# Optimization experiments

Hardware: AMD Instinct MI355X
Metric: run time of the kernel (lower is better)

## Reference

```python
import jax, jax.numpy as jnp
import numpy as np

B, S = 16384, 2048
EPS = 1e-8


def _autocorr(x, lag):
    # Pearson correlation between x[:, :-lag] and x[:, lag:] (ddof cancels).
    a = x[:, :-lag]
    b = x[:, lag:]
    am = a.mean(axis=1, keepdims=True)
    bm = b.mean(axis=1, keepdims=True)
    cov = ((a - am) * (b - bm)).mean(axis=1)
    return cov / (a.std(axis=1) * b.std(axis=1))


def _stat_features(x):
    S_len = x.shape[1]
    mean = x.mean(axis=1)
    xc = x - mean[:, None]
    m2 = (xc ** 2).mean(axis=1)
    m3 = (xc ** 3).mean(axis=1)
    m4 = (xc ** 4).mean(axis=1)
    std = jnp.sqrt(m2)
    min_v = x.min(axis=1)
    max_v = x.max(axis=1)
    q = jnp.percentile(x, jnp.array([25.0, 50.0, 75.0]), axis=1)  # [3, B]
    p25, median, p75 = q[0], q[1], q[2]
    diff = jnp.diff(x, axis=1)
    std_diff = diff.std(axis=1)
    trend = std_diff / (std + EPS)
    ac1 = _autocorr(x, 1)
    ac7 = _autocorr(x, 7)
    ac24 = _autocorr(x, 24)
    cv = std / (jnp.abs(mean) + EPS)
    iqr = p75 - p25
    seasonal = x[:, ::24].var(axis=1) / (m2 + EPS)
    skew = m3 / (m2 ** 1.5)          # scipy.stats.skew, bias=True
    kurt = m4 / (m2 ** 2) - 3.0      # scipy.stats.kurtosis, Fisher, bias=True
    length = jnp.full_like(mean, float(S_len))
    sum_abs_diff = jnp.abs(diff).sum(axis=1)
    mean_abs_diff = jnp.abs(diff).mean(axis=1)
    feats = jnp.stack([mean, std, min_v, max_v, median, trend, ac1, ac7, ac24,
                       cv, iqr, seasonal, skew, kurt, length,
                       sum_abs_diff, mean_abs_diff, std_diff, p25, p75], axis=1)
    return jnp.where(jnp.isfinite(feats), feats, 0.0)


def setup_inputs() -> dict:
    key = jax.random.key(0)
    k0, k1, k2, k3, k4 = jax.random.split(key, 5)
    x = jax.random.normal(k0, (B, S), dtype=jnp.float32)
    W1 = jax.random.normal(k1, (64, 20), dtype=jnp.float32) * 0.1
    b1 = jnp.zeros((64,), dtype=jnp.float32)
    W2 = jax.random.normal(k3, (128, 64), dtype=jnp.float32) * 0.1
    b2 = jnp.zeros((128,), dtype=jnp.float32)
    return {"x": x, "W1": W1, "b1": b1, "W2": W2, "b2": b2}


def reference(x, W1, b1, W2, b2):
    feats = _stat_features(x)                      # [B, 20]
    h = jax.nn.relu(feats @ W1.T + b1)             # [B, 64] (dropout inactive at eval)
    return h @ W2.T + b2                           # [B, 128]
```

## Files before the change

kernel.cpp:

```cpp
#include <hip/hip_runtime.h>
#include <cmath>

constexpr int S_LEN = 2048;
constexpr float EPS = 1e-8f;

typedef unsigned uvec32 __attribute__((ext_vector_type(32)));

__device__ __forceinline__ float fin(float v) { return isfinite(v) ? v : 0.0f; }

__device__ __forceinline__ unsigned f2o_bits(unsigned u) {
    return (u & 0x80000000u) ? ~u : (u | 0x80000000u);
}
__device__ __forceinline__ float o2f(unsigned u) {
    return __uint_as_float((u & 0x80000000u) ? (u ^ 0x80000000u) : ~u);
}

template <int Ctrl, int Rmask>
__device__ __forceinline__ int dpp_zero_i(int x) {
    return __builtin_amdgcn_update_dpp(0, x, Ctrl, Rmask, 0xF, true);
}
template <int Ctrl>
__device__ __forceinline__ int dpp_keep_i(int x) {
    return __builtin_amdgcn_update_dpp(x, x, Ctrl, 0xF, 0xF, false);
}
__device__ __forceinline__ int wred_add_i(int v) {
    v += dpp_zero_i<0xB1, 0xF>(v);
    v += dpp_zero_i<0x4E, 0xF>(v);
    v += dpp_zero_i<0x114, 0xF>(v);
    v += dpp_zero_i<0x118, 0xF>(v);
    v += dpp_zero_i<0x142, 0xA>(v);
    v += dpp_zero_i<0x143, 0xC>(v);
    return __builtin_amdgcn_readlane(v, 63);
}
__device__ __forceinline__ float wred_add_f(float v) {
    #define ADDF(CT, RM) v += __uint_as_float((unsigned)dpp_zero_i<CT, RM>((int)__float_as_uint(v)))
    ADDF(0xB1, 0xF); ADDF(0x4E, 0xF); ADDF(0x114, 0xF);
    ADDF(0x118, 0xF); ADDF(0x142, 0xA); ADDF(0x143, 0xC);
    #undef ADDF
    return __uint_as_float((unsigned)__builtin_amdgcn_readlane((int)__float_as_uint(v), 63));
}
__device__ __forceinline__ float wred_min_f(float v) {
    #define MINF(CT) v = fminf(v, __uint_as_float((unsigned)dpp_keep_i<CT>((int)__float_as_uint(v))))
    MINF(0xB1); MINF(0x4E); MINF(0x114); MINF(0x118); MINF(0x142); MINF(0x143);
    #undef MINF
    return __uint_as_float((unsigned)__builtin_amdgcn_readlane((int)__float_as_uint(v), 63));
}
__device__ __forceinline__ float wred_max_f(float v) {
    #define MAXF(CT) v = fmaxf(v, __uint_as_float((unsigned)dpp_keep_i<CT>((int)__float_as_uint(v))))
    MAXF(0xB1); MAXF(0x4E); MAXF(0x114); MAXF(0x118); MAXF(0x142); MAXF(0x143);
    #undef MAXF
    return __uint_as_float((unsigned)__builtin_amdgcn_readlane((int)__float_as_uint(v), 63));
}
__device__ __forceinline__ unsigned wred_umin(unsigned v) {
    #define MINU(CT) { unsigned t = (unsigned)dpp_keep_i<CT>((int)v); v = v < t ? v : t; }
    MINU(0xB1) MINU(0x4E) MINU(0x114) MINU(0x118) MINU(0x142) MINU(0x143)
    #undef MINU
    return (unsigned)__builtin_amdgcn_readlane((int)v, 63);
}
__device__ __forceinline__ float readlane_f(float x, int l) {
    return __uint_as_float((unsigned)__builtin_amdgcn_readlane((int)__float_as_uint(x), l));
}

__device__ __forceinline__ void transpose32(uvec32& A) {
    #pragma unroll
    for (int j = 16; j; j >>= 1) {
        unsigned m = (j == 16) ? 0x0000FFFFu : (j == 8) ? 0x00FF00FFu
                   : (j == 4) ? 0x0F0F0F0Fu : (j == 2) ? 0x33333333u : 0x55555555u;
        #pragma unroll
        for (int k = 0; k < 32; k++) {
            if (!(k & j)) {
                unsigned t = (A[k] ^ (A[k | j] >> j)) & m;
                A[k] = A[k] ^ t;
                A[k | j] = A[k | j] ^ (t << j);
            }
        }
    }
}

#define VF(e) __uint_as_float(a[e])

__global__ __launch_bounds__(256) void transpose_w_kernel(
    const float* __restrict__ W1, const float* __restrict__ W2, float* __restrict__ wt)
{
    int tid = blockIdx.x * blockDim.x + threadIdx.x;
    int stride = gridDim.x * blockDim.x;
    for (int n = tid; n < 64 * 20; n += stride) {
        int j = n & 63, k = n >> 6;
        wt[n] = W1[j * 20 + k];
    }
    for (int n = tid; n < 128 * 64; n += stride) {
        int o = n & 127, k = n >> 7;
        wt[1280 + n] = W2[o * 64 + k];
    }
}

__global__ __launch_bounds__(256) void fused_stats_mlp_kernel(
    const float* __restrict__ x, const float* __restrict__ wt,
    const float* __restrict__ b1, const float* __restrict__ b2,
    float* __restrict__ out, int nrows)
{
    __shared__ __align__(16) float sf[4][20];
    __shared__ __align__(16) float hsh[4][64];

    const int gw   = (blockIdx.x * 256 + threadIdx.x) >> 6;
    const int lane = threadIdx.x & 63;
    const int w    = (threadIdx.x >> 6);
    if (gw >= nrows) return;

    uvec32 a;
    const float* xr = x + (size_t)gw * S_LEN + lane * 32;
    #pragma unroll
    for (int q = 0; q < 8; q++) {
        float4 t = reinterpret_cast<const float4*>(xr)[q];
        a[4 * q + 0] = __float_as_uint(t.x); a[4 * q + 1] = __float_as_uint(t.y);
        a[4 * q + 2] = __float_as_uint(t.z); a[4 * q + 3] = __float_as_uint(t.w);
    }

    float s1 = 0.f, s2 = 0.f, sd2 = 0.f, sad = 0.f;
    float p1 = 0.f, p7 = 0.f, p24 = 0.f, se1 = 0.f, se2 = 0.f;
    float mn = VF(0), mx = VF(0);
    #pragma unroll
    for (int e = 0; e < 32; e++) {
        float val = VF(e);
        s1 += val; s2 = fmaf(val, val, s2);
        mn = fminf(mn, val); mx = fmaxf(mx, val);
    }
    #pragma unroll
    for (int e = 0; e < 31; e++) {
        float d = VF(e + 1) - VF(e);
        sd2 = fmaf(d, d, sd2); sad += fabsf(d);
        p1 = fmaf(VF(e), VF(e + 1), p1);
    }
    #pragma unroll
    for (int e = 0; e < 25; e++) p7 = fmaf(VF(e), VF(e + 7), p7);
    #pragma unroll
    for (int e = 0; e < 8; e++)  p24 = fmaf(VF(e), VF(e + 24), p24);

    const bool notlast = (lane < 63);
    #pragma unroll
    for (int j = 0; j < 24; j++) {
        float nb = __shfl_down(VF(j), 1, 64);
        float g = notlast ? nb : 0.f;
        p24 = fmaf(VF(8 + j), g, p24);
        if (j < 7) p7 = fmaf(VF(25 + j), g, p7);
        if (j == 0 && notlast) {
            float d = nb - VF(31);
            sd2 = fmaf(d, d, sd2); sad += fabsf(d);
            p1 = fmaf(VF(31), nb, p1);
        }
    }
    {
        int r3 = lane % 3;
        float sv = (r3 == 0) ? VF(0) : ((r3 == 1) ? VF(16) : VF(8));
        se1 += sv; se2 = fmaf(sv, sv, se2);
        if (r3 == 0) { se1 += VF(24); se2 = fmaf(VF(24), VF(24), se2); }
    }
    float aa = 0, bb = 0, h7v = 0, hq7v = 0;
    #pragma unroll
    for (int e = 0; e < 24; e++) {
        aa += VF(e); bb = fmaf(VF(e), VF(e), bb);
        if (e == 6) { h7v = aa; hq7v = bb; }
    }
    float cc = 0, dd = 0, t7v = 0, tq7v = 0;
    #pragma unroll
    for (int e = 31; e >= 8; e--) {
        cc += VF(e); dd = fmaf(VF(e), VF(e), dd);
        if (e == 25) { t7v = cc; tq7v = dd; }
    }
    const float h1  = readlane_f(VF(0), 0),   t1  = readlane_f(VF(31), 63);
    const float h7  = readlane_f(h7v, 0),     hq7 = readlane_f(hq7v, 0);
    const float h24 = readlane_f(aa, 0),      hq24 = readlane_f(bb, 0);
    const float t7  = readlane_f(t7v, 63),    tq7 = readlane_f(tq7v, 63);
    const float t24 = readlane_f(cc, 63),     tq24 = readlane_f(dd, 63);
    const float hq1 = h1 * h1, tq1 = t1 * t1;

    float S1  = wred_add_f(s1);
    float mean = S1 * (1.0f / S_LEN);
    float S2  = wred_add_f(s2);
    float SD2 = wred_add_f(sd2);
    float SAD = wred_add_f(sad);
    float P1  = wred_add_f(p1);
    float P7  = wred_add_f(p7);
    float P24 = wred_add_f(p24);
    float SE1 = wred_add_f(se1);
    float SE2 = wred_add_f(se2);
    float MN  = wred_min_f(mn);
    float MX  = wred_max_f(mx);

    float c2 = 0.f, c3 = 0.f, c4 = 0.f;
    #pragma unroll
    for (int e = 0; e < 32; e++) {
        float xc = VF(e) - mean;
        float q = xc * xc;
        c2 += q; c3 = fmaf(q, xc, c3); c4 = fmaf(q, q, c4);
    }
    float C2 = wred_add_f(c2), C3 = wred_add_f(c3), C4 = wred_add_f(c4);

    {
        const float Sf = (float)S_LEN;
        const float nd = Sf - 1.0f;
        float m2v = C2 / Sf, m3v = C3 / Sf, m4v = C4 / Sf;
        float stdv = sqrtf(m2v);
        float dmean = (t1 - h1) / nd;
        float dvar = SD2 / nd - dmean * dmean;
        float std_diff = sqrtf(fmaxf(dvar, 0.f));
        float trend = std_diff / (stdv + EPS);
        float ac[3];
        const float Ls[3] = {1.f, 7.f, 24.f};
        const float Ps[3] = {P1, P7, P24};
        const float hd[3] = {h1, h7, h24},   hqv[3] = {hq1, hq7, hq24};
        const float tl[3] = {t1, t7, t24},   tqv[3] = {tq1, tq7, tq24};
        #pragma unroll
        for (int q = 0; q < 3; q++) {
            float n = Sf - Ls[q];
            float sa = S1 - tl[q], sb = S1 - hd[q];
            float qa = S2 - tqv[q], qb = S2 - hqv[q];
            float am = sa / n, bm = sb / n;
            float cov = Ps[q] / n - am * bm;
            float as_ = sqrtf(fmaxf(qa / n - am * am, 0.f));
            float bs_ = sqrtf(fmaxf(qb / n - bm * bm, 0.f));
            ac[q] = cov / (as_ * bs_);
        }
        float cv = stdv / (fabsf(mean) + EPS);
        float sm = SE1 / 86.f;
        float svar = SE2 / 86.f - sm * sm;
        float seasonal = svar / (m2v + EPS);
        float skew = m3v / (m2v * stdv);
        float kurt = m4v / (m2v * m2v) - 3.f;
        if (lane == 0) {
            float* s = sf[w];
            s[0]  = fin(mean);     s[1]  = fin(stdv);
            s[2]  = fin(MN);       s[3]  = fin(MX);
            s[5]  = fin(trend);    s[6]  = fin(ac[0]);
            s[7]  = fin(ac[1]);    s[8]  = fin(ac[2]);
            s[9]  = fin(cv);       s[11] = fin(seasonal);
            s[12] = fin(skew);     s[13] = fin(kurt);
            s[14] = Sf;            s[15] = fin(SAD);
            s[16] = fin(SAD / nd); s[17] = fin(std_diff);
        }
    }

    #pragma unroll
    for (int e = 0; e < 32; e++) a[e] = f2o_bits(a[e]);
    transpose32(a);

    unsigned act0 = ~0u, act1 = ~0u, act2 = ~0u;
    int K0 = 511, K1 = 1023, K2 = 1535;
    unsigned uK0 = 0, uK1 = 0, uK2 = 0;
    #pragma unroll
    for (int b = 31; b >= 0; b--) {
        unsigned mb = a[31 - b];
        unsigned nmb = ~mb;
        unsigned z0 = act0 & nmb, z1 = act1 & nmb, z2 = act2 & nmb;
        int C01 = wred_add_i(__popc(z0) | (__popc(z1) << 16));
        int Cc2 = wred_add_i(__popc(z2));
        int c0 = C01 & 0xFFFF;
        int c1 = (int)((unsigned)C01 >> 16);
        if (K0 < c0)  act0 = z0; else { K0 -= c0;  act0 &= mb; uK0 |= (1u << b); }
        if (K1 < c1)  act1 = z1; else { K1 -= c1;  act1 &= mb; uK1 |= (1u << b); }
        if (K2 < Cc2) act2 = z2; else { K2 -= Cc2; act2 &= mb; uK2 |= (1u << b); }
    }
    int e01 = wred_add_i(__popc(act0) | (__popc(act1) << 16));
    int eq0 = e01 & 0xFFFF, eq1 = (int)((unsigned)e01 >> 16);
    int eq2 = wred_add_i(__popc(act2));

    transpose32(a);
    unsigned m0 = ~0u, m1 = ~0u, m2 = ~0u;
    #pragma unroll
    for (int e = 0; e < 32; e++) {
        unsigned ue = a[e];
        if (ue > uK0) m0 = m0 < ue ? m0 : ue;
        if (ue > uK1) m1 = m1 < ue ? m1 : ue;
        if (ue > uK2) m2 = m2 < ue ? m2 : ue;
    }
    m0 = wred_umin(m0); m1 = wred_umin(m1); m2 = wred_umin(m2);

    float v511 = o2f(uK0), v1023 = o2f(uK1), v1535 = o2f(uK2);
    float v512  = (K0 + 1 < eq0) ? v511  : o2f(m0);
    float v1024 = (K1 + 1 < eq1) ? v1023 : o2f(m1);
    float v1536 = (K2 + 1 < eq2) ? v1535 : o2f(m2);
    float p25 = v511 + 0.75f * (v512 - v511);
    float med = 0.5f * (v1023 + v1024);
    float p75 = v1535 + 0.25f * (v1536 - v1535);
    float iqr = p75 - p25;

    if (lane == 0) {
        float* s = sf[w];
        s[4]  = fin(med); s[10] = fin(iqr);
        s[18] = fin(p25); s[19] = fin(p75);
    }
    __asm__ volatile("s_waitcnt lgkmcnt(0)" ::: "memory");
    __builtin_amdgcn_sched_barrier(0);

    const float* W1T = wt;
    const float* W2T = wt + 1280;
    const float4* sfv = (const float4*)sf[w];
    float4 f0 = sfv[0], f1 = sfv[1], f2 = sfv[2], f3 = sfv[3], f4 = sfv[4];
    float h = b1[lane];
    h = fmaf(f0.x, W1T[ 0 * 64 + lane], h);
    h = fmaf(f0.y, W1T[ 1 * 64 + lane], h);
    h = fmaf(f0.z, W1T[ 2 * 64 + lane], h);
    h = fmaf(f0.w, W1T[ 3 * 64 + lane], h);
    h = fmaf(f1.x, W1T[ 4 * 64 + lane], h);
    h = fmaf(f1.y, W1T[ 5 * 64 + lane], h);
    h = fmaf(f1.z, W1T[ 6 * 64 + lane], h);
    h = fmaf(f1.w, W1T[ 7 * 64 + lane], h);
    h = fmaf(f2.x, W1T[ 8 * 64 + lane], h);
    h = fmaf(f2.y, W1T[ 9 * 64 + lane], h);
    h = fmaf(f2.z, W1T[10 * 64 + lane], h);
    h = fmaf(f2.w, W1T[11 * 64 + lane], h);
    h = fmaf(f3.x, W1T[12 * 64 + lane], h);
    h = fmaf(f3.y, W1T[13 * 64 + lane], h);
    h = fmaf(f3.z, W1T[14 * 64 + lane], h);
    h = fmaf(f3.w, W1T[15 * 64 + lane], h);
    h = fmaf(f4.x, W1T[16 * 64 + lane], h);
    h = fmaf(f4.y, W1T[17 * 64 + lane], h);
    h = fmaf(f4.z, W1T[18 * 64 + lane], h);
    h = fmaf(f4.w, W1T[19 * 64 + lane], h);
    h = fmaxf(h, 0.f);
    hsh[w][lane] = h;
    __asm__ volatile("s_waitcnt lgkmcnt(0)" ::: "memory");
    __builtin_amdgcn_sched_barrier(0);

    const int j2 = lane * 2;
    float2 b2v = *(const float2*)(b2 + j2);
    float acc0 = b2v.x, acc1 = b2v.y;
    const float4* hv4 = (const float4*)hsh[w];
    #pragma unroll
    for (int q = 0; q < 16; q++) {
        float4 hq = hv4[q];
        const float* wp = W2T + (4 * q) * 128 + j2;
        float2 w0 = *(const float2*)(wp);
        float2 w1 = *(const float2*)(wp + 128);
        float2 w2 = *(const float2*)(wp + 256);
        float2 w3 = *(const float2*)(wp + 384);
        acc0 = fmaf(hq.x, w0.x, acc0); acc1 = fmaf(hq.x, w0.y, acc1);
        acc0 = fmaf(hq.y, w1.x, acc0); acc1 = fmaf(hq.y, w1.y, acc1);
        acc0 = fmaf(hq.z, w2.x, acc0); acc1 = fmaf(hq.z, w2.y, acc1);
        acc0 = fmaf(hq.w, w3.x, acc0); acc1 = fmaf(hq.w, w3.y, acc1);
    }
    *(float2*)(out + (size_t)gw * 128 + j2) = make_float2(acc0, acc1);
}

extern "C" void kernel_launch(void* const* d_in, const int* in_sizes, int n_in,
                              void* d_out, int out_size, void* d_ws, size_t ws_size,
                              hipStream_t stream) {
    const float* x  = (const float*)d_in[0];
    const float* W1 = (const float*)d_in[1];
    const float* b1 = (const float*)d_in[2];
    const float* W2 = (const float*)d_in[3];
    const float* b2 = (const float*)d_in[4];
    float* out = (float*)d_out;
    float* wt  = (float*)d_ws;
    int nrows = in_sizes[0] / S_LEN;
    int blocks = (nrows + 3) / 4;
    transpose_w_kernel<<<8, 256, 0, stream>>>(W1, W2, wt);
    fused_stats_mlp_kernel<<<blocks, 256, 0, stream>>>(x, wt, b1, b2, out, nrows);
}
```

Baseline: 274.5 us.

## Speed up bit transpose, radix select, divisions and W2 access in fused kernel

Replaces the first two stages of the 32x32 bit transpose with byte-permute instructions and reworks the radix-select loop to count ones and track remaining counts, which removes the trailing equality reductions. Replaces the guarded min with a wrapped unsigned subtract. Swaps divisions for reciprocal multiplies using hardware rcp, reads W2 directly row-wise as float4 so its transpose is dropped from the prep kernel, and adds an occupancy hint to launch bounds. The rcp approximation may change results slightly.

```diff
diff --git a/kernel.cpp b/kernel.cpp
--- a/kernel.cpp
+++ b/kernel.cpp
@@ -7,6 +7,7 @@
 typedef unsigned uvec32 __attribute__((ext_vector_type(32)));
 
 __device__ __forceinline__ float fin(float v) { return isfinite(v) ? v : 0.0f; }
+__device__ __forceinline__ float rcpf(float x) { return __builtin_amdgcn_rcpf(x); }
 
 __device__ __forceinline__ unsigned f2o_bits(unsigned u) {
     return (u & 0x80000000u) ? ~u : (u | 0x80000000u);
@@ -63,9 +64,23 @@
 
 __device__ __forceinline__ void transpose32(uvec32& A) {
     #pragma unroll
-    for (int j = 16; j; j >>= 1) {
-        unsigned m = (j == 16) ? 0x0000FFFFu : (j == 8) ? 0x00FF00FFu
-                   : (j == 4) ? 0x0F0F0F0Fu : (j == 2) ? 0x33333333u : 0x55555555u;
+    for (int k = 0; k < 16; k++) {
+        unsigned lo = __builtin_amdgcn_perm(A[k], A[k + 16], 0x07060302u);
+        unsigned hi = __builtin_amdgcn_perm(A[k], A[k + 16], 0x05040100u);
+        A[k] = lo; A[k + 16] = hi;
+    }
+    #pragma unroll
+    for (int k0 = 0; k0 < 32; k0 += 16) {
+        #pragma unroll
+        for (int k = k0; k < k0 + 8; k++) {
+            unsigned lo = __builtin_amdgcn_perm(A[k], A[k + 8], 0x07030501u);
+            unsigned hi = __builtin_amdgcn_perm(A[k], A[k + 8], 0x06020400u);
+            A[k] = lo; A[k + 8] = hi;
+        }
+    }
+    #pragma unroll
+    for (int j = 4; j; j >>= 1) {
+        unsigned m = (j == 4) ? 0x0F0F0F0Fu : (j == 2) ? 0x33333333u : 0x55555555u;
         #pragma unroll
         for (int k = 0; k < 32; k++) {
             if (!(k & j)) {
@@ -80,7 +95,7 @@
 #define VF(e) __uint_as_float(a[e])
 
 __global__ __launch_bounds__(256) void transpose_w_kernel(
-    const float* __restrict__ W1, const float* __restrict__ W2, float* __restrict__ wt)
+    const float* __restrict__ W1, float* __restrict__ wt)
 {
     int tid = blockIdx.x * blockDim.x + threadIdx.x;
     int stride = gridDim.x * blockDim.x;
@@ -88,16 +103,12 @@
         int j = n & 63, k = n >> 6;
         wt[n] = W1[j * 20 + k];
     }
-    for (int n = tid; n < 128 * 64; n += stride) {
-        int o = n & 127, k = n >> 7;
-        wt[1280 + n] = W2[o * 64 + k];
-    }
-}
-
-__global__ __launch_bounds__(256) void fused_stats_mlp_kernel(
+}
+
+__global__ __launch_bounds__(256, 4) void fused_stats_mlp_kernel(
     const float* __restrict__ x, const float* __restrict__ wt,
-    const float* __restrict__ b1, const float* __restrict__ b2,
-    float* __restrict__ out, int nrows)
+    const float* __restrict__ b1, const float* __restrict__ W2,
+    const float* __restrict__ b2, float* __restrict__ out, int nrows)
 {
     __shared__ __align__(16) float sf[4][20];
     __shared__ __align__(16) float hsh[4][64];
@@ -197,36 +208,37 @@
     float C2 = wred_add_f(c2), C3 = wred_add_f(c3), C4 = wred_add_f(c4);
 
     {
+        constexpr float invS  = 1.0f / 2048.0f;
+        constexpr float invND = 1.0f / 2047.0f;
         const float Sf = (float)S_LEN;
-        const float nd = Sf - 1.0f;
-        float m2v = C2 / Sf, m3v = C3 / Sf, m4v = C4 / Sf;
+        float m2v = C2 * invS, m3v = C3 * invS, m4v = C4 * invS;
         float stdv = sqrtf(m2v);
-        float dmean = (t1 - h1) / nd;
-        float dvar = SD2 / nd - dmean * dmean;
+        float dmean = (t1 - h1) * invND;
+        float dvar = SD2 * invND - dmean * dmean;
         float std_diff = sqrtf(fmaxf(dvar, 0.f));
-        float trend = std_diff / (stdv + EPS);
+        float trend = std_diff * rcpf(stdv + EPS);
         float ac[3];
-        const float Ls[3] = {1.f, 7.f, 24.f};
+        const float invN[3] = {1.0f / 2047.0f, 1.0f / 2041.0f, 1.0f / 2024.0f};
         const float Ps[3] = {P1, P7, P24};
         const float hd[3] = {h1, h7, h24},   hqv[3] = {hq1, hq7, hq24};
         const float tl[3] = {t1, t7, t24},   tqv[3] = {tq1, tq7, tq24};
         #pragma unroll
         for (int q = 0; q < 3; q++) {
-            float n = Sf - Ls[q];
+            float in = invN[q];
             float sa = S1 - tl[q], sb = S1 - hd[q];
             float qa = S2 - tqv[q], qb = S2 - hqv[q];
-            float am = sa / n, bm = sb / n;
-            float cov = Ps[q] / n - am * bm;
-            float as_ = sqrtf(fmaxf(qa / n - am * am, 0.f));
-            float bs_ = sqrtf(fmaxf(qb / n - bm * bm, 0.f));
-            ac[q] = cov / (as_ * bs_);
-        }
-        float cv = stdv / (fabsf(mean) + EPS);
-        float sm = SE1 / 86.f;
-        float svar = SE2 / 86.f - sm * sm;
-        float seasonal = svar / (m2v + EPS);
-        float skew = m3v / (m2v * stdv);
-        float kurt = m4v / (m2v * m2v) - 3.f;
+            float am = sa * in, bm = sb * in;
+            float cov = Ps[q] * in - am * bm;
+            float as_ = sqrtf(fmaxf(qa * in - am * am, 0.f));
+            float bs_ = sqrtf(fmaxf(qb * in - bm * bm, 0.f));
+            ac[q] = cov * rcpf(as_ * bs_);
+        }
+        float cv = stdv * rcpf(fabsf(mean) + EPS);
+        float sm = SE1 * (1.0f / 86.0f);
+        float svar = SE2 * (1.0f / 86.0f) - sm * sm;
+        float seasonal = svar * rcpf(m2v + EPS);
+        float skew = m3v * rcpf(m2v * stdv);
+        float kurt = m4v * rcpf(m2v * m2v) - 3.f;
         if (lane == 0) {
             float* s = sf[w];
             s[0]  = fin(mean);     s[1]  = fin(stdv);
@@ -236,7 +248,7 @@
             s[9]  = fin(cv);       s[11] = fin(seasonal);
             s[12] = fin(skew);     s[13] = fin(kurt);
             s[14] = Sf;            s[15] = fin(SAD);
-            s[16] = fin(SAD / nd); s[17] = fin(std_diff);
+            s[16] = fin(SAD * invND); s[17] = fin(std_diff);
         }
     }
 
@@ -246,34 +258,36 @@
 
     unsigned act0 = ~0u, act1 = ~0u, act2 = ~0u;
     int K0 = 511, K1 = 1023, K2 = 1535;
+    int cnt0 = 2048, cnt1 = 2048, cnt2 = 2048;
     unsigned uK0 = 0, uK1 = 0, uK2 = 0;
     #pragma unroll
     for (int b = 31; b >= 0; b--) {
         unsigned mb = a[31 - b];
-        unsigned nmb = ~mb;
-        unsigned z0 = act0 & nmb, z1 = act1 & nmb, z2 = act2 & nmb;
-        int C01 = wred_add_i(__popc(z0) | (__popc(z1) << 16));
-        int Cc2 = wred_add_i(__popc(z2));
-        int c0 = C01 & 0xFFFF;
-        int c1 = (int)((unsigned)C01 >> 16);
-        if (K0 < c0)  act0 = z0; else { K0 -= c0;  act0 &= mb; uK0 |= (1u << b); }
-        if (K1 < c1)  act1 = z1; else { K1 -= c1;  act1 &= mb; uK1 |= (1u << b); }
-        if (K2 < Cc2) act2 = z2; else { K2 -= Cc2; act2 &= mb; uK2 |= (1u << b); }
-    }
-    int e01 = wred_add_i(__popc(act0) | (__popc(act1) << 16));
-    int eq0 = e01 & 0xFFFF, eq1 = (int)((unsigned)e01 >> 16);
-    int eq2 = wred_add_i(__popc(act2));
+        unsigned w0 = act0 & mb, w1 = act1 & mb, w2 = act2 & mb;
+        int O01 = wred_add_i(__popc(w0) | (__popc(w1) << 16));
+        int O2  = wred_add_i(__popc(w2));
+        int c0 = cnt0 - (O01 & 0xFFFF);
+        int c1 = cnt1 - (int)((unsigned)O01 >> 16);
+        int c2i = cnt2 - O2;
+        if (K0 < c0)  { act0 ^= w0; cnt0 = c0; }  else { K0 -= c0;  act0 = w0; cnt0 -= c0;  uK0 |= (1u << b); }
+        if (K1 < c1)  { act1 ^= w1; cnt1 = c1; }  else { K1 -= c1;  act1 = w1; cnt1 -= c1;  uK1 |= (1u << b); }
+        if (K2 < c2i) { act2 ^= w2; cnt2 = c2i; } else { K2 -= c2i; act2 = w2; cnt2 -= c2i; uK2 |= (1u << b); }
+    }
+    const int eq0 = cnt0, eq1 = cnt1, eq2 = cnt2;
 
     transpose32(a);
+    const unsigned k0p1 = uK0 + 1, k1p1 = uK1 + 1, k2p1 = uK2 + 1;
     unsigned m0 = ~0u, m1 = ~0u, m2 = ~0u;
     #pragma unroll
     for (int e = 0; e < 32; e++) {
         unsigned ue = a[e];
-        if (ue > uK0) m0 = m0 < ue ? m0 : ue;
-        if (ue > uK1) m1 = m1 < ue ? m1 : ue;
-        if (ue > uK2) m2 = m2 < ue ? m2 : ue;
-    }
-    m0 = wred_umin(m0); m1 = wred_umin(m1); m2 = wred_umin(m2);
+        unsigned d0 = ue - k0p1; m0 = m0 < d0 ? m0 : d0;
+        unsigned d1 = ue - k1p1; m1 = m1 < d1 ? m1 : d1;
+        unsigned d2 = ue - k2p1; m2 = m2 < d2 ? m2 : d2;
+    }
+    m0 = wred_umin(m0) + k0p1;
+    m1 = wred_umin(m1) + k1p1;
+    m2 = wred_umin(m2) + k2p1;
 
     float v511 = o2f(uK0), v1023 = o2f(uK1), v1535 = o2f(uK2);
     float v512  = (K0 + 1 < eq0) ? v511  : o2f(m0);
@@ -293,7 +307,6 @@
     __builtin_amdgcn_sched_barrier(0);
 
     const float* W1T = wt;
-    const float* W2T = wt + 1280;
     const float4* sfv = (const float4*)sf[w];
     float4 f0 = sfv[0], f1 = sfv[1], f2 = sfv[2], f3 = sfv[3], f4 = sfv[4];
     float h = b1[lane];
@@ -325,19 +338,18 @@
     const int j2 = lane * 2;
     float2 b2v = *(const float2*)(b2 + j2);
     float acc0 = b2v.x, acc1 = b2v.y;
+    const float4* w2r0 = (const float4*)(W2 + (size_t)j2 * 64);
+    const float4* w2r1 = (const float4*)(W2 + (size_t)(j2 + 1) * 64);
     const float4* hv4 = (const float4*)hsh[w];
     #pragma unroll
     for (int q = 0; q < 16; q++) {
         float4 hq = hv4[q];
-        const float* wp = W2T + (4 * q) * 128 + j2;
-        float2 w0 = *(const float2*)(wp);
-        float2 w1 = *(const float2*)(wp + 128);
-        float2 w2 = *(const float2*)(wp + 256);
-        float2 w3 = *(const float2*)(wp + 384);
-        acc0 = fmaf(hq.x, w0.x, acc0); acc1 = fmaf(hq.x, w0.y, acc1);
-        acc0 = fmaf(hq.y, w1.x, acc0); acc1 = fmaf(hq.y, w1.y, acc1);
-        acc0 = fmaf(hq.z, w2.x, acc0); acc1 = fmaf(hq.z, w2.y, acc1);
-        acc0 = fmaf(hq.w, w3.x, acc0); acc1 = fmaf(hq.w, w3.y, acc1);
+        float4 wa = w2r0[q];
+        float4 wb = w2r1[q];
+        acc0 = fmaf(hq.x, wa.x, acc0); acc1 = fmaf(hq.x, wb.x, acc1);
+        acc0 = fmaf(hq.y, wa.y, acc0); acc1 = fmaf(hq.y, wb.y, acc1);
+        acc0 = fmaf(hq.z, wa.z, acc0); acc1 = fmaf(hq.z, wb.z, acc1);
+        acc0 = fmaf(hq.w, wa.w, acc0); acc1 = fmaf(hq.w, wb.w, acc1);
     }
     *(float2*)(out + (size_t)gw * 128 + j2) = make_float2(acc0, acc1);
 }
@@ -354,6 +366,6 @@
     float* wt  = (float*)d_ws;
     int nrows = in_sizes[0] / S_LEN;
     int blocks = (nrows + 3) / 4;
-    transpose_w_kernel<<<8, 256, 0, stream>>>(W1, W2, wt);
-    fused_stats_mlp_kernel<<<blocks, 256, 0, stream>>>(x, wt, b1, b2, out, nrows);
-}
+    transpose_w_kernel<<<2, 256, 0, stream>>>(W1, wt);
+    fused_stats_mlp_kernel<<<blocks, 256, 0, stream>>>(x, wt, b1, W2, b2, out, nrows);
+}
```

Measured after the change: 267.7 us. 2.5% less time.
